# Optimization experiments

Hardware: AMD Instinct MI355X
Metric: run time of the kernel (lower is better)

Reference implementation:

```python
import jax, jax.numpy as jnp
import numpy as np

B, S = 512, 64
ZD, GD, SK = 256, 16, 512   # vel_z_dim, genre_cond_dim, skel_encode_dim
H = 1024                    # vel_hidden_dim
ND, VC = 9, 4               # n_drum_classes, vel_cond_dim


def _gru(x, h, Wi, Wh, bi, bh):
    # torch.nn.GRUCell math; gates ordered [r, z, n]
    gi = x @ Wi.T + bi
    gh = h @ Wh.T + bh
    i_r, i_z, i_n = jnp.split(gi, 3, axis=-1)
    h_r, h_z, h_n = jnp.split(gh, 3, axis=-1)
    r = jax.nn.sigmoid(i_r + h_r)
    zg = jax.nn.sigmoid(i_z + h_z)
    n = jnp.tanh(i_n + r * h_n)
    return (1.0 - zg) * n + zg * h


def setup_inputs() -> dict:
    key = jax.random.key(0)
    ks = jax.random.split(key, 14)
    rn = lambda k, shp, s: jax.random.normal(k, shp, dtype=jnp.float32) * s
    return dict(
        z=rn(ks[0], (B, ZD), 1.0),
        note_encoded=rn(ks[1], (B, SK), 1.0),
        vel_target=jax.random.uniform(ks[2], (B, S, ND), dtype=jnp.float32),
        note=jax.random.uniform(ks[3], (B, S, ND), dtype=jnp.float32),
        vel_cond=jax.random.uniform(ks[4], (B, S, VC), dtype=jnp.float32),
        genre_cond=rn(ks[5], (B, GD), 1.0),
        W_in=rn(ks[6], (H, ZD + SK + GD), 0.02), b_in=jnp.zeros((H,), jnp.float32),
        W_ih1=rn(ks[7], (3 * H, ND * 2 + VC), 0.05), W_hh1=rn(ks[8], (3 * H, H), 0.02),
        b_ih1=jnp.zeros((3 * H,), jnp.float32), b_hh1=jnp.zeros((3 * H,), jnp.float32),
        W_ih2=rn(ks[9], (3 * H, H), 0.02), W_hh2=rn(ks[10], (3 * H, H), 0.02),
        b_ih2=jnp.zeros((3 * H,), jnp.float32), b_hh2=jnp.zeros((3 * H,), jnp.float32),
        W_out=rn(ks[11], (ND, H), 0.02), b_out=jnp.zeros((ND,), jnp.float32),
        training=0, teacher_forcing_ratio=0,
    )


def reference(z, note_encoded, vel_target, note, vel_cond, genre_cond,
              W_in, b_in, W_ih1, W_hh1, b_ih1, b_hh1,
              W_ih2, W_hh2, b_ih2, b_hh2, W_out, b_out,
              training, teacher_forcing_ratio):
    # eval mode: dropout = identity, teacher forcing never taken
    del vel_target, training, teacher_forcing_ratio
    bsz = z.shape[0]
    zc = jnp.concatenate([z.reshape(bsz, -1), note_encoded, genre_cond], axis=-1)
    h1 = jnp.tanh(zc @ W_in.T + b_in)              # [B, H]
    h2 = jnp.zeros_like(h1)                        # overwritten at step 0
    out0 = jnp.zeros((bsz, W_out.shape[0]), z.dtype)

    def step(carry, xs):
        out, h1, h2 = carry
        i, nt, ct = xs
        inp = jnp.concatenate([out, nt, ct], axis=-1)       # [B, 2*ND+VC]
        h1 = _gru(inp, h1, W_ih1, W_hh1, b_ih1, b_hh1)
        h2 = jnp.where(i == 0, h1, h2)                      # hx[1] = hx[0] at i==0
        h2 = _gru(h1, h2, W_ih2, W_hh2, b_ih2, b_hh2)
        vel = jax.nn.sigmoid(h2 @ W_out.T + b_out)          # [B, ND]
        return (vel, h1, h2), vel

    xs = (jnp.arange(note.shape[1]),
          jnp.transpose(note, (1, 0, 2)),
          jnp.transpose(vel_cond, (1, 0, 2)))
    _, outs = jax.lax.scan(step, (out0, h1, h2), xs)
    return jnp.transpose(outs, (1, 0, 2))                    # [B, S, ND]
```

## Files before the change

kernel.cpp:

```cpp
#include <hip/hip_runtime.h>
#include <hip/hip_bf16.h>

#define HD 1024
#define BB 512
#define SS 64
#define N3 3072
#define NC 9216
#define ND 9
#define VC 4
#define KI 832

typedef __attribute__((ext_vector_type(8))) short bf16x8;
typedef __attribute__((ext_vector_type(4))) float f32x4;

__device__ __forceinline__ ushort f2b(float f) {
    unsigned u = __builtin_bit_cast(unsigned, f);
    u += 0x7fffu + ((u >> 16) & 1u);
    return (ushort)(u >> 16);
}

__device__ __forceinline__ float sigf(float x) {
    return 1.f / (1.f + __expf(-x));
}

__device__ __forceinline__ void gld_lds16(const void* g, void* l) {
    __builtin_amdgcn_global_load_lds(
        (const __attribute__((address_space(1))) unsigned int*)g,
        (__attribute__((address_space(3))) unsigned int*)l, 16, 0, 0);
}

__global__ __launch_bounds__(256) void prep_w(
    const float* __restrict__ Wih2, const float* __restrict__ Whh1,
    const float* __restrict__ Whh2, ushort* __restrict__ Wcat)
{
    const int row = blockIdx.x;
    const float* src = row < 3072 ? Wih2 + (size_t)row * HD
                     : row < 6144 ? Whh1 + (size_t)(row - 3072) * HD
                                  : Whh2 + (size_t)(row - 6144) * HD;
    const int c = threadIdx.x * 4;
    float4 v = *(const float4*)(src + c);
    ushort4 o;
    o.x = f2b(v.x); o.y = f2b(v.y); o.z = f2b(v.z); o.w = f2b(v.w);
    *(ushort4*)(Wcat + (size_t)row * HD + c) = o;
}

__global__ __launch_bounds__(256) void prep_wt1(
    const float* __restrict__ Wih1, float* __restrict__ Wt1)
{
    const int g = blockIdx.x * 256 + threadIdx.x;
    #pragma unroll
    for (int c = 0; c < 22; ++c)
        Wt1[c * N3 + g] = Wih1[(size_t)g * 22 + c];
}

__global__ __launch_bounds__(256) void prep_acat(
    const float* __restrict__ z, const float* __restrict__ ne,
    const float* __restrict__ gc, ushort* __restrict__ Acat)
{
    const int b = blockIdx.x;
    const int t = threadIdx.x;
    if (t >= 208) return;
    const int c = t * 4;
    float4 v = make_float4(0.f, 0.f, 0.f, 0.f);
    if (c < 256)      v = *(const float4*)(z  + (size_t)b * 256 + c);
    else if (c < 768) v = *(const float4*)(ne + (size_t)b * 512 + (c - 256));
    else if (c < 784) v = *(const float4*)(gc + (size_t)b * 16  + (c - 768));
    ushort4 o;
    o.x = f2b(v.x); o.y = f2b(v.y); o.z = f2b(v.z); o.w = f2b(v.w);
    *(ushort4*)(Acat + (size_t)b * KI + c) = o;
}

__global__ __launch_bounds__(256) void prep_win(
    const float* __restrict__ W_in, ushort* __restrict__ W_inb)
{
    const int r = blockIdx.x;
    const int t = threadIdx.x;
    if (t >= 208) return;
    const int c = t * 4;
    ushort4 o = {0, 0, 0, 0};
    if (c < 784) {
        float4 v = *(const float4*)(W_in + (size_t)r * 784 + c);
        o.x = f2b(v.x); o.y = f2b(v.y); o.z = f2b(v.z); o.w = f2b(v.w);
    }
    *(ushort4*)(W_inb + (size_t)r * KI + c) = o;
}

__global__ __launch_bounds__(256) void k_init(
    const ushort* __restrict__ Acat, const ushort* __restrict__ W_inb,
    const float* __restrict__ b_in, float* __restrict__ h1, ushort* __restrict__ h1b)
{
    __shared__ __align__(16) ushort As[2 * 4096];
    __shared__ __align__(16) ushort Bs[2 * 4096];
    const int t = blockIdx.x;
    const int nt = t >> 3, mt = t & 7;

    const int tid = threadIdx.x;
    const int w = tid >> 6, l = tid & 63;
    const int lr = l >> 3;
    const int sw = ((l & 7) ^ lr) << 3;

    const ushort* Ag0 = Acat + ((size_t)(mt << 6)) * KI + (size_t)(16 * w + lr) * KI + sw;
    const ushort* Ag1 = Ag0 + 8 * KI;
    const ushort* Bg0 = W_inb + ((size_t)(nt << 6)) * KI + (size_t)(16 * w + lr) * KI + sw;
    const ushort* Bg1 = Bg0 + 8 * KI;
    const int o0 = (16 * w) * 64, o1 = (16 * w + 8) * 64;

    gld_lds16(Ag0, As + o0); gld_lds16(Ag1, As + o1);
    gld_lds16(Bg0, Bs + o0); gld_lds16(Bg1, Bs + o1);

    const int wm = (w >> 1) << 5, wn = (w & 1) << 5;
    const int fr = l & 15, fc = l >> 4;
    const int ra0 = wm + fr, ra1 = wm + 16 + fr;
    const int rb0 = wn + fr, rb1 = wn + 16 + fr;

    f32x4 acc[2][2] = {};
    for (int kt = 0; kt < 13; ++kt) {
        const int cb = (kt & 1) << 12;
        __syncthreads();
        if (kt + 1 < 13) {
            const int nb = ((kt + 1) & 1) << 12;
            const int ko = (kt + 1) << 6;
            gld_lds16(Ag0 + ko, As + nb + o0);
            gld_lds16(Ag1 + ko, As + nb + o1);
            gld_lds16(Bg0 + ko, Bs + nb + o0);
            gld_lds16(Bg1 + ko, Bs + nb + o1);
        }
        #pragma unroll
        for (int kk = 0; kk < 2; ++kk) {
            const int c = (kk << 2) + fc;
            bf16x8 a0 = *(const bf16x8*)(As + cb + ra0 * 64 + ((c ^ (ra0 & 7)) << 3));
            bf16x8 a1 = *(const bf16x8*)(As + cb + ra1 * 64 + ((c ^ (ra1 & 7)) << 3));
            bf16x8 b0 = *(const bf16x8*)(Bs + cb + rb0 * 64 + ((c ^ (rb0 & 7)) << 3));
            bf16x8 b1 = *(const bf16x8*)(Bs + cb + rb1 * 64 + ((c ^ (rb1 & 7)) << 3));
            acc[0][0] = __builtin_amdgcn_mfma_f32_16x16x32_bf16(a0, b0, acc[0][0], 0, 0, 0);
            acc[0][1] = __builtin_amdgcn_mfma_f32_16x16x32_bf16(a0, b1, acc[0][1], 0, 0, 0);
            acc[1][0] = __builtin_amdgcn_mfma_f32_16x16x32_bf16(a1, b0, acc[1][0], 0, 0, 0);
            acc[1][1] = __builtin_amdgcn_mfma_f32_16x16x32_bf16(a1, b1, acc[1][1], 0, 0, 0);
        }
    }

    const int row0 = (mt << 6) + wm;
    const int col0 = (nt << 6) + wn + fr;
    const float b0v = b_in[col0], b1v = b_in[col0 + 16];
    #pragma unroll
    for (int i = 0; i < 2; ++i) {
        #pragma unroll
        for (int r = 0; r < 4; ++r) {
            const int row = row0 + i * 16 + fc * 4 + r;
            const float v0 = tanhf(acc[i][0][r] + b0v);
            const float v1 = tanhf(acc[i][1][r] + b1v);
            h1[(size_t)row * HD + col0]       = v0;
            h1b[(size_t)row * HD + col0]      = f2b(v0);
            h1[(size_t)row * HD + col0 + 16]  = v1;
            h1b[(size_t)row * HD + col0 + 16] = f2b(v1);
        }
    }
}

__global__ __launch_bounds__(256) void gemm3(
    const ushort* __restrict__ h1b, const ushort* __restrict__ h2b,
    const ushort* __restrict__ Wcat, float* __restrict__ Cbuf, int ntb)
{
    __shared__ __align__(16) ushort As[4096];
    __shared__ __align__(16) ushort Ws[4096];

    const int flat = blockIdx.x + (blockIdx.y << 3);
    const int id   = (flat & 7) * gridDim.y + (flat >> 3);
    const int bm   = (id & 7) << 6;
    const int nt   = (id >> 3) + ntb;

    const ushort* Amat = (nt < 96) ? h1b : h2b;
    const ushort* W    = Wcat + (size_t)(nt << 6) * HD;

    const int tid = threadIdx.x;
    const int w   = tid >> 6;
    const int l   = tid & 63;

    const int srow = l >> 3;
    const int sch  = ((l & 7) ^ srow) << 3;
    const ushort* Ag0 = Amat + (size_t)(bm + 16 * w + srow) * HD + sch;
    const ushort* Ag1 = Ag0 + 8 * HD;
    const ushort* Wg0 = W + (size_t)(16 * w + srow) * HD + sch;
    const ushort* Wg1 = Wg0 + 8 * HD;
    ushort* Al0 = As + (16 * w) * 64;
    ushort* Al1 = As + (16 * w + 8) * 64;
    ushort* Wl0 = Ws + (16 * w) * 64;
    ushort* Wl1 = Ws + (16 * w + 8) * 64;

    const int wm = (w >> 1) << 5;
    const int wn = (w & 1) << 5;
    const int fr = l & 15;
    const int fc = l >> 4;

    const int ra0 = wm + fr,  ra1 = wm + 16 + fr;
    const int rb0 = wn + fr,  rb1 = wn + 16 + fr;

    f32x4 acc00 = {0.f,0.f,0.f,0.f}, acc01 = {0.f,0.f,0.f,0.f};
    f32x4 acc10 = {0.f,0.f,0.f,0.f}, acc11 = {0.f,0.f,0.f,0.f};

    for (int kt = 0; kt < 16; ++kt) {
        const int ko = kt << 6;
        __syncthreads();
        gld_lds16(Ag0 + ko, Al0);
        gld_lds16(Ag1 + ko, Al1);
        gld_lds16(Wg0 + ko, Wl0);
        gld_lds16(Wg1 + ko, Wl1);
        __syncthreads();
        #pragma unroll
        for (int kk = 0; kk < 2; ++kk) {
            const int c = (kk << 2) + fc;
            bf16x8 a0 = *(const bf16x8*)(As + ra0 * 64 + ((c ^ (ra0 & 7)) << 3));
            bf16x8 a1 = *(const bf16x8*)(As + ra1 * 64 + ((c ^ (ra1 & 7)) << 3));
            bf16x8 b0 = *(const bf16x8*)(Ws + rb0 * 64 + ((c ^ (rb0 & 7)) << 3));
            bf16x8 b1 = *(const bf16x8*)(Ws + rb1 * 64 + ((c ^ (rb1 & 7)) << 3));
            acc00 = __builtin_amdgcn_mfma_f32_16x16x32_bf16(a0, b0, acc00, 0, 0, 0);
            acc01 = __builtin_amdgcn_mfma_f32_16x16x32_bf16(a0, b1, acc01, 0, 0, 0);
            acc10 = __builtin_amdgcn_mfma_f32_16x16x32_bf16(a1, b0, acc10, 0, 0, 0);
            acc11 = __builtin_amdgcn_mfma_f32_16x16x32_bf16(a1, b1, acc11, 0, 0, 0);
        }
    }

    const int bn = nt << 6;
    float* Cw = Cbuf + (size_t)(bm + wm) * NC + bn + wn;
    #pragma unroll
    for (int r = 0; r < 4; ++r) {
        const size_t ro0 = (size_t)(fc * 4 + r) * NC;
        const size_t ro1 = (size_t)(16 + fc * 4 + r) * NC;
        Cw[ro0 + fr]      = acc00[r];
        Cw[ro0 + 16 + fr] = acc01[r];
        Cw[ro1 + fr]      = acc10[r];
        Cw[ro1 + 16 + fr] = acc11[r];
    }
}

__global__ __launch_bounds__(1024) void gru1_first(
    const float* __restrict__ Cbuf, float* __restrict__ h1, ushort* __restrict__ h1b,
    float* __restrict__ h2, ushort* __restrict__ h2b,
    const float* __restrict__ note, const float* __restrict__ velc,
    const float* __restrict__ Wt1, const float* __restrict__ b_ih1,
    const float* __restrict__ b_hh1)
{
    __shared__ float inp[22];
    const int b = blockIdx.x;
    const int j = threadIdx.x;

    if (j < 22) {
        float v = 0.f;
        if (j >= 9 && j < 18) v = note[(size_t)b * (SS * ND) + (j - 9)];
        else if (j >= 18)     v = velc[(size_t)b * (SS * VC) + (j - 18)];
        inp[j] = v;
    }
    __syncthreads();

    float ir = b_ih1[j], iz = b_ih1[HD + j], inn = b_ih1[2 * HD + j];
    #pragma unroll
    for (int c = 0; c < 22; ++c) {
        const float x = inp[c];
        const float* wr = Wt1 + c * N3;
        ir  = fmaf(x, wr[j],          ir);
        iz  = fmaf(x, wr[HD + j],     iz);
        inn = fmaf(x, wr[2 * HD + j], inn);
    }

    const float* g = Cbuf + (size_t)b * NC + N3;
    const float hr = g[j]          + b_hh1[j];
    const float hz = g[HD + j]     + b_hh1[HD + j];
    const float hn = g[2 * HD + j] + b_hh1[2 * HD + j];

    const float rg = sigf(ir + hr);
    const float zg = sigf(iz + hz);
    const float n  = tanhf(inn + rg * hn);
    const float hnew = (1.f - zg) * n + zg * h1[(size_t)b * HD + j];
    const ushort hb = f2b(hnew);
    h1[(size_t)b * HD + j]  = hnew;
    h1b[(size_t)b * HD + j] = hb;
    h2[(size_t)b * HD + j]  = hnew;
    h2b[(size_t)b * HD + j] = hb;
}

__global__ __launch_bounds__(1024) void pw_fused(
    const float* __restrict__ Cbuf, float* __restrict__ h1, ushort* __restrict__ h1b,
    float* __restrict__ h2, ushort* __restrict__ h2b,
    const float* __restrict__ note, const float* __restrict__ velc,
    const float* __restrict__ Wt1,
    const float* __restrict__ b_ih1, const float* __restrict__ b_hh1,
    const float* __restrict__ b_ih2, const float* __restrict__ b_hh2,
    const float* __restrict__ W_out, const float* __restrict__ b_out,
    float* __restrict__ dout, int step)
{
    __shared__ float hs[HD];
    __shared__ float inp[22];
    const int b = blockIdx.x;
    const int j = threadIdx.x;

    if (step + 1 < SS && j >= 9 && j < 22) {
        inp[j] = (j < 18) ? note[(size_t)b * (SS * ND) + (step + 1) * ND + (j - 9)]
                          : velc[(size_t)b * (SS * VC) + (step + 1) * VC + (j - 18)];
    }

    const float* gi = Cbuf + (size_t)b * NC;
    const float* gh = gi + 2 * N3;

    const float ir  = gi[j]          + b_ih2[j];
    const float hr  = gh[j]          + b_hh2[j];
    const float iz  = gi[HD + j]     + b_ih2[HD + j];
    const float hz  = gh[HD + j]     + b_hh2[HD + j];
    const float inn = gi[2 * HD + j] + b_ih2[2 * HD + j];
    const float hn  = gh[2 * HD + j] + b_hh2[2 * HD + j];

    const float rg = sigf(ir + hr);
    const float zg = sigf(iz + hz);
    const float n  = tanhf(inn + rg * hn);
    const float hnew = (1.f - zg) * n + zg * h2[(size_t)b * HD + j];
    h2[(size_t)b * HD + j]  = hnew;
    h2b[(size_t)b * HD + j] = f2b(hnew);
    hs[j] = hnew;
    __syncthreads();

    const int w = j >> 6;
    const int t = j & 63;
    if (w < ND) {
        float a = 0.f;
        const float* wr = W_out + (size_t)w * HD;
        #pragma unroll
        for (int k = 0; k < HD / 64; ++k)
            a = fmaf(hs[t + k * 64], wr[t + k * 64], a);
        #pragma unroll
        for (int off = 32; off > 0; off >>= 1) a += __shfl_down(a, off);
        if (t == 0) {
            const float o = sigf(a + b_out[w]);
            dout[(size_t)b * (SS * ND) + step * ND + w] = o;
            inp[w] = o;
        }
    }
    __syncthreads();

    if (step + 1 < SS) {
        float xir = b_ih1[j], xiz = b_ih1[HD + j], xinn = b_ih1[2 * HD + j];
        #pragma unroll
        for (int c = 0; c < 22; ++c) {
            const float x = inp[c];
            const float* wr = Wt1 + c * N3;
            xir  = fmaf(x, wr[j],          xir);
            xiz  = fmaf(x, wr[HD + j],     xiz);
            xinn = fmaf(x, wr[2 * HD + j], xinn);
        }
        const float* g1 = Cbuf + (size_t)b * NC + N3;
        const float hr1 = g1[j]          + b_hh1[j];
        const float hz1 = g1[HD + j]     + b_hh1[HD + j];
        const float hn1 = g1[2 * HD + j] + b_hh1[2 * HD + j];

        const float rg1 = sigf(xir + hr1);
        const float zg1 = sigf(xiz + hz1);
        const float n1  = tanhf(xinn + rg1 * hn1);
        const float h1new = (1.f - zg1) * n1 + zg1 * h1[(size_t)b * HD + j];
        h1[(size_t)b * HD + j]  = h1new;
        h1b[(size_t)b * HD + j] = f2b(h1new);
    }
}

extern "C" void kernel_launch(void* const* d_in, const int* in_sizes, int n_in,
                              void* d_out, int out_size, void* d_ws, size_t ws_size,
                              hipStream_t stream)
{
    const float* z     = (const float*)d_in[0];
    const float* ne    = (const float*)d_in[1];
    const float* note  = (const float*)d_in[3];
    const float* velc  = (const float*)d_in[4];
    const float* gc    = (const float*)d_in[5];
    const float* W_in  = (const float*)d_in[6];
    const float* b_in  = (const float*)d_in[7];
    const float* W_ih1 = (const float*)d_in[8];
    const float* W_hh1 = (const float*)d_in[9];
    const float* b_ih1 = (const float*)d_in[10];
    const float* b_hh1 = (const float*)d_in[11];
    const float* W_ih2 = (const float*)d_in[12];
    const float* W_hh2 = (const float*)d_in[13];
    const float* b_ih2 = (const float*)d_in[14];
    const float* b_hh2 = (const float*)d_in[15];
    const float* W_out = (const float*)d_in[16];
    const float* b_out = (const float*)d_in[17];
    float* out = (float*)d_out;

    float*  h1   = (float*)d_ws;
    float*  h2   = h1 + BB * HD;
    float*  Cbuf = h2 + BB * HD;
    float*  Wt1  = Cbuf + (size_t)BB * NC;
    ushort* h1b  = (ushort*)(Wt1 + 22 * N3);
    ushort* h2b  = h1b + BB * HD;
    ushort* Wcat = h2b + BB * HD;
    ushort* Acat  = (ushort*)Cbuf;
    ushort* W_inb = Acat + (size_t)BB * KI;

    prep_w   <<<dim3(NC), 256, 0, stream>>>(W_ih2, W_hh1, W_hh2, Wcat);
    prep_wt1 <<<dim3(12), 256, 0, stream>>>(W_ih1, Wt1);
    prep_acat<<<dim3(BB), 256, 0, stream>>>(z, ne, gc, Acat);
    prep_win <<<dim3(HD), 256, 0, stream>>>(W_in, W_inb);

    k_init<<<dim3(128), 256, 0, stream>>>(Acat, W_inb, b_in, h1, h1b);

    gemm3<<<dim3(8, 48), 256, 0, stream>>>(h1b, h2b, Wcat, Cbuf, 48);
    gru1_first<<<dim3(BB), 1024, 0, stream>>>(Cbuf, h1, h1b, h2, h2b,
                                              note, velc, Wt1, b_ih1, b_hh1);

    for (int s = 0; s < SS; ++s) {
        gemm3<<<dim3(8, 144), 256, 0, stream>>>(h1b, h2b, Wcat, Cbuf, 0);
        pw_fused<<<dim3(BB), 1024, 0, stream>>>(Cbuf, h1, h1b, h2, h2b,
                                                note, velc, Wt1,
                                                b_ih1, b_hh1, b_ih2, b_hh2,
                                                W_out, b_out, out, s);
    }
}
```

Measured before the change: 2.094 ms.

## Double-buffer LDS tiles in gemm3 with K-tile 32 and prefetch

Restructures the gemm3 main loop to use two LDS buffers with 32-wide K tiles. The next tile's global-to-LDS load is issued while the current tile is fed to MFMA, and there is now one barrier per iteration instead of two. The goal is to hide global load latency behind compute. In exchange the iteration count doubles and each iteration does less MFMA work to cover the barrier cost. The XOR swizzle is adapted to the narrower rows.

```diff
diff --git a/kernel.cpp b/kernel.cpp
--- a/kernel.cpp
+++ b/kernel.cpp
@@ -161,8 +161,8 @@
     const ushort* __restrict__ h1b, const ushort* __restrict__ h2b,
     const ushort* __restrict__ Wcat, float* __restrict__ Cbuf, int ntb)
 {
-    __shared__ __align__(16) ushort As[4096];
-    __shared__ __align__(16) ushort Ws[4096];
+    __shared__ __align__(16) ushort As[2 * 2048];
+    __shared__ __align__(16) ushort Ws[2 * 2048];
 
     const int flat = blockIdx.x + (blockIdx.y << 3);
     const int id   = (flat & 7) * gridDim.y + (flat >> 3);
@@ -176,16 +176,12 @@
     const int w   = tid >> 6;
     const int l   = tid & 63;
 
-    const int srow = l >> 3;
-    const int sch  = ((l & 7) ^ srow) << 3;
-    const ushort* Ag0 = Amat + (size_t)(bm + 16 * w + srow) * HD + sch;
-    const ushort* Ag1 = Ag0 + 8 * HD;
-    const ushort* Wg0 = W + (size_t)(16 * w + srow) * HD + sch;
-    const ushort* Wg1 = Wg0 + 8 * HD;
-    ushort* Al0 = As + (16 * w) * 64;
-    ushort* Al1 = As + (16 * w + 8) * 64;
-    ushort* Wl0 = Ws + (16 * w) * 64;
-    ushort* Wl1 = Ws + (16 * w + 8) * 64;
+    const int srow = l >> 2;
+    const int sch  = ((l & 3) ^ (srow & 3)) << 3;
+    const ushort* Ag = Amat + (size_t)(bm + 16 * w + srow) * HD + sch;
+    const ushort* Wg = W    + (size_t)(16 * w + srow) * HD + sch;
+    ushort* Al = As + (w << 9);
+    ushort* Wl = Ws + (w << 9);
 
     const int wm = (w >> 1) << 5;
     const int wn = (w & 1) << 5;
@@ -194,30 +190,34 @@
 
     const int ra0 = wm + fr,  ra1 = wm + 16 + fr;
     const int rb0 = wn + fr,  rb1 = wn + 16 + fr;
+    const int oa0 = ra0 * 32 + ((fc ^ (ra0 & 3)) << 3);
+    const int oa1 = ra1 * 32 + ((fc ^ (ra1 & 3)) << 3);
+    const int ob0 = rb0 * 32 + ((fc ^ (rb0 & 3)) << 3);
+    const int ob1 = rb1 * 32 + ((fc ^ (rb1 & 3)) << 3);
 
     f32x4 acc00 = {0.f,0.f,0.f,0.f}, acc01 = {0.f,0.f,0.f,0.f};
     f32x4 acc10 = {0.f,0.f,0.f,0.f}, acc11 = {0.f,0.f,0.f,0.f};
 
-    for (int kt = 0; kt < 16; ++kt) {
-        const int ko = kt << 6;
+    gld_lds16(Ag, Al);
+    gld_lds16(Wg, Wl);
+
+    for (int kt = 0; kt < 32; ++kt) {
+        const int cb = (kt & 1) << 11;
         __syncthreads();
-        gld_lds16(Ag0 + ko, Al0);
-        gld_lds16(Ag1 + ko, Al1);
-        gld_lds16(Wg0 + ko, Wl0);
-        gld_lds16(Wg1 + ko, Wl1);
-        __syncthreads();
-        #pragma unroll
-        for (int kk = 0; kk < 2; ++kk) {
-            const int c = (kk << 2) + fc;
-            bf16x8 a0 = *(const bf16x8*)(As + ra0 * 64 + ((c ^ (ra0 & 7)) << 3));
-            bf16x8 a1 = *(const bf16x8*)(As + ra1 * 64 + ((c ^ (ra1 & 7)) << 3));
-            bf16x8 b0 = *(const bf16x8*)(Ws + rb0 * 64 + ((c ^ (rb0 & 7)) << 3));
-            bf16x8 b1 = *(const bf16x8*)(Ws + rb1 * 64 + ((c ^ (rb1 & 7)) << 3));
-            acc00 = __builtin_amdgcn_mfma_f32_16x16x32_bf16(a0, b0, acc00, 0, 0, 0);
-            acc01 = __builtin_amdgcn_mfma_f32_16x16x32_bf16(a0, b1, acc01, 0, 0, 0);
-            acc10 = __builtin_amdgcn_mfma_f32_16x16x32_bf16(a1, b0, acc10, 0, 0, 0);
-            acc11 = __builtin_amdgcn_mfma_f32_16x16x32_bf16(a1, b1, acc11, 0, 0, 0);
-        }
+        if (kt < 31) {
+            const int nb = ((kt + 1) & 1) << 11;
+            const int ko = (kt + 1) << 5;
+            gld_lds16(Ag + ko, Al + nb);
+            gld_lds16(Wg + ko, Wl + nb);
+        }
+        bf16x8 a0 = *(const bf16x8*)(As + cb + oa0);
+        bf16x8 a1 = *(const bf16x8*)(As + cb + oa1);
+        bf16x8 b0 = *(const bf16x8*)(Ws + cb + ob0);
+        bf16x8 b1 = *(const bf16x8*)(Ws + cb + ob1);
+        acc00 = __builtin_amdgcn_mfma_f32_16x16x32_bf16(a0, b0, acc00, 0, 0, 0);
+        acc01 = __builtin_amdgcn_mfma_f32_16x16x32_bf16(a0, b1, acc01, 0, 0, 0);
+        acc10 = __builtin_amdgcn_mfma_f32_16x16x32_bf16(a1, b0, acc10, 0, 0, 0);
+        acc11 = __builtin_amdgcn_mfma_f32_16x16x32_bf16(a1, b1, acc11, 0, 0, 0);
     }
 
     const int bn = nt << 6;
```

Result: slower. 2.503 ms (+19.5%).
